# Performance work log

Measured on AMD Instinct MI355X. Metric: run time of the kernel, lower is better.

Reference implementation:

```python
import jax, jax.numpy as jnp
import numpy as np

NUM_CLASSES = 32768
FEAT_DIM = 512
BATCH = 1024


def setup_inputs() -> dict:
    key = jax.random.key(0)
    k1, k2, k3 = jax.random.split(key, 3)
    x = jax.random.normal(k1, (BATCH, FEAT_DIM), dtype=jnp.float32)
    labels = jax.random.randint(k2, (BATCH,), 0, NUM_CLASSES, dtype=jnp.int64)
    centers = jax.random.normal(k3, (NUM_CLASSES, FEAT_DIM), dtype=jnp.float32)
    return {"x": x, "labels": labels, "centers": centers}


def reference(x, labels, centers):
    # Original computes full cdist(x, centers)**2 / 2 and masks to the
    # label-matched column; mathematically identical to gathering each
    # sample's own center and taking half the squared L2 distance.
    c = centers[labels]                       # [B, D] gather
    diff = x - c                              # [B, D]
    per_sample = 0.5 * jnp.sum(diff * diff, axis=1)  # [B]
    return jnp.mean(per_sample)               # reduction='mean'
```

## Files before the change

kernel.cpp:

```cpp
#include <hip/hip_runtime.h>

#define BATCH 1024
#define FEAT_DIM 512
#define NBLK 128
#define MAGIC 0x5CA1AB1Eu

__global__ __launch_bounds__(256) void cl_fused(
    const float* __restrict__ x,
    const int* __restrict__ labels,
    const float* __restrict__ centers,
    float* __restrict__ partial,
    unsigned int* __restrict__ flags,
    float* __restrict__ out)
{
    const int wave = threadIdx.x >> 6;
    const int lane = threadIdx.x & 63;
    const int b0   = blockIdx.x * 8 + wave * 2;
    const int b1   = b0 + 1;

    const int lab0 = labels[b0];
    const int lab1 = labels[b1];

    const float4* __restrict__ x0 =
        reinterpret_cast<const float4*>(x + (size_t)b0 * FEAT_DIM);
    const float4* __restrict__ x1 =
        reinterpret_cast<const float4*>(x + (size_t)b1 * FEAT_DIM);
    const float4* __restrict__ c0 =
        reinterpret_cast<const float4*>(centers + (size_t)lab0 * FEAT_DIM);
    const float4* __restrict__ c1 =
        reinterpret_cast<const float4*>(centers + (size_t)lab1 * FEAT_DIM);

    const float4 xa = x0[lane];
    const float4 xb = x0[lane + 64];
    const float4 xc = x1[lane];
    const float4 xd = x1[lane + 64];
    const float4 ca = c0[lane];
    const float4 cb = c0[lane + 64];
    const float4 cc = c1[lane];
    const float4 cd = c1[lane + 64];

    float s;
    {
        const float e0 = xa.x - ca.x, e1 = xa.y - ca.y;
        const float e2 = xa.z - ca.z, e3 = xa.w - ca.w;
        const float e4 = xb.x - cb.x, e5 = xb.y - cb.y;
        const float e6 = xb.z - cb.z, e7 = xb.w - cb.w;
        const float f0 = xc.x - cc.x, f1 = xc.y - cc.y;
        const float f2 = xc.z - cc.z, f3 = xc.w - cc.w;
        const float f4 = xd.x - cd.x, f5 = xd.y - cd.y;
        const float f6 = xd.z - cd.z, f7 = xd.w - cd.w;
        s = e0 * e0 + e1 * e1 + e2 * e2 + e3 * e3
          + e4 * e4 + e5 * e5 + e6 * e6 + e7 * e7
          + f0 * f0 + f1 * f1 + f2 * f2 + f3 * f3
          + f4 * f4 + f5 * f5 + f6 * f6 + f7 * f7;
    }

    #pragma unroll
    for (int off = 32; off > 0; off >>= 1)
        s += __shfl_down(s, off, 64);

    __shared__ float wsum[4];
    if (lane == 0) wsum[wave] = s;
    __syncthreads();

    if (threadIdx.x == 0) {
        const float p = wsum[0] + wsum[1] + wsum[2] + wsum[3];
        __hip_atomic_store(&partial[blockIdx.x], p,
                           __ATOMIC_RELAXED, __HIP_MEMORY_SCOPE_AGENT);
        __hip_atomic_store(&flags[blockIdx.x], MAGIC,
                           __ATOMIC_RELEASE, __HIP_MEMORY_SCOPE_AGENT);
    }

    if (blockIdx.x == 0 && wave == 0) {
        const int i0 = lane, i1 = lane + 64;
        bool done = false;
        while (!__all(done)) {
            done = (__hip_atomic_load(&flags[i0], __ATOMIC_ACQUIRE,
                                      __HIP_MEMORY_SCOPE_AGENT) == MAGIC)
                && (__hip_atomic_load(&flags[i1], __ATOMIC_ACQUIRE,
                                      __HIP_MEMORY_SCOPE_AGENT) == MAGIC);
            if (!done) __builtin_amdgcn_s_sleep(2);
        }

        float t = __hip_atomic_load(&partial[i0], __ATOMIC_RELAXED,
                                    __HIP_MEMORY_SCOPE_AGENT)
                + __hip_atomic_load(&partial[i1], __ATOMIC_RELAXED,
                                    __HIP_MEMORY_SCOPE_AGENT);

        #pragma unroll
        for (int off = 32; off > 0; off >>= 1)
            t += __shfl_down(t, off, 64);

        if (lane == 0) out[0] = t * (0.5f / (float)BATCH);

        __hip_atomic_store(&flags[i0], 0u, __ATOMIC_RELAXED, __HIP_MEMORY_SCOPE_AGENT);
        __hip_atomic_store(&flags[i1], 0u, __ATOMIC_RELAXED, __HIP_MEMORY_SCOPE_AGENT);
    }
}

extern "C" void kernel_launch(void* const* d_in, const int* in_sizes, int n_in,
                              void* d_out, int out_size, void* d_ws, size_t ws_size,
                              hipStream_t stream) {
    const float* x       = (const float*)d_in[0];
    const int*   labels  = (const int*)d_in[1];
    const float* centers = (const float*)d_in[2];
    float*       out     = (float*)d_out;

    float*        partial = (float*)d_ws;
    unsigned int* flags   = (unsigned int*)((char*)d_ws + 1024);

    cl_fused<<<NBLK, 256, 0, stream>>>(x, labels, centers, partial, flags, out);
}
```

Before: 10.38 us.

## Use dedicated reducer block and 64 worker blocks with four samples per wave

```diff
diff --git a/kernel.cpp b/kernel.cpp
--- a/kernel.cpp
+++ b/kernel.cpp
@@ -2,7 +2,7 @@
 
 #define BATCH 1024
 #define FEAT_DIM 512
-#define NBLK 128
+#define NWORK 64
 #define MAGIC 0x5CA1AB1Eu
 
 __global__ __launch_bounds__(256) void cl_fused(
@@ -15,44 +15,85 @@
 {
     const int wave = threadIdx.x >> 6;
     const int lane = threadIdx.x & 63;
-    const int b0   = blockIdx.x * 8 + wave * 2;
-    const int b1   = b0 + 1;
+
+    if (blockIdx.x == 0) {
+        if (wave == 0) {
+            bool done = false;
+            while (!__all(done)) {
+                done = (__hip_atomic_load(&flags[lane], __ATOMIC_RELAXED,
+                                          __HIP_MEMORY_SCOPE_AGENT) == MAGIC);
+            }
+            __builtin_amdgcn_fence(__ATOMIC_ACQUIRE, "agent");
+
+            float t = __hip_atomic_load(&partial[lane], __ATOMIC_RELAXED,
+                                        __HIP_MEMORY_SCOPE_AGENT);
+            #pragma unroll
+            for (int off = 32; off > 0; off >>= 1)
+                t += __shfl_down(t, off, 64);
+
+            if (lane == 0) out[0] = t * (0.5f / (float)BATCH);
+
+            __hip_atomic_store(&flags[lane], 0u, __ATOMIC_RELAXED,
+                               __HIP_MEMORY_SCOPE_AGENT);
+        }
+        return;
+    }
+
+    const int blk = blockIdx.x - 1;
+    const int b0  = blk * 16 + wave * 4;
 
     const int lab0 = labels[b0];
-    const int lab1 = labels[b1];
+    const int lab1 = labels[b0 + 1];
+    const int lab2 = labels[b0 + 2];
+    const int lab3 = labels[b0 + 3];
 
-    const float4* __restrict__ x0 =
+    const float4* __restrict__ xr =
         reinterpret_cast<const float4*>(x + (size_t)b0 * FEAT_DIM);
-    const float4* __restrict__ x1 =
-        reinterpret_cast<const float4*>(x + (size_t)b1 * FEAT_DIM);
     const float4* __restrict__ c0 =
         reinterpret_cast<const float4*>(centers + (size_t)lab0 * FEAT_DIM);
     const float4* __restrict__ c1 =
         reinterpret_cast<const float4*>(centers + (size_t)lab1 * FEAT_DIM);
+    const float4* __restrict__ c2 =
+        reinterpret_cast<const float4*>(centers + (size_t)lab2 * FEAT_DIM);
+    const float4* __restrict__ c3 =
+        reinterpret_cast<const float4*>(centers + (size_t)lab3 * FEAT_DIM);
 
-    const float4 xa = x0[lane];
-    const float4 xb = x0[lane + 64];
-    const float4 xc = x1[lane];
-    const float4 xd = x1[lane + 64];
-    const float4 ca = c0[lane];
-    const float4 cb = c0[lane + 64];
-    const float4 cc = c1[lane];
-    const float4 cd = c1[lane + 64];
+    const float4 xa0 = xr[lane];
+    const float4 xa1 = xr[lane + 64];
+    const float4 xb0 = xr[lane + 128];
+    const float4 xb1 = xr[lane + 192];
+    const float4 xc0 = xr[lane + 256];
+    const float4 xc1 = xr[lane + 320];
+    const float4 xd0 = xr[lane + 384];
+    const float4 xd1 = xr[lane + 448];
+    const float4 ca0 = c0[lane];
+    const float4 ca1 = c0[lane + 64];
+    const float4 cb0 = c1[lane];
+    const float4 cb1 = c1[lane + 64];
+    const float4 cc0 = c2[lane];
+    const float4 cc1 = c2[lane + 64];
+    const float4 cd0 = c3[lane];
+    const float4 cd1 = c3[lane + 64];
 
-    float s;
+    float s = 0.f;
     {
-        const float e0 = xa.x - ca.x, e1 = xa.y - ca.y;
-        const float e2 = xa.z - ca.z, e3 = xa.w - ca.w;
-        const float e4 = xb.x - cb.x, e5 = xb.y - cb.y;
-        const float e6 = xb.z - cb.z, e7 = xb.w - cb.w;
-        const float f0 = xc.x - cc.x, f1 = xc.y - cc.y;
-        const float f2 = xc.z - cc.z, f3 = xc.w - cc.w;
-        const float f4 = xd.x - cd.x, f5 = xd.y - cd.y;
-        const float f6 = xd.z - cd.z, f7 = xd.w - cd.w;
-        s = e0 * e0 + e1 * e1 + e2 * e2 + e3 * e3
-          + e4 * e4 + e5 * e5 + e6 * e6 + e7 * e7
-          + f0 * f0 + f1 * f1 + f2 * f2 + f3 * f3
-          + f4 * f4 + f5 * f5 + f6 * f6 + f7 * f7;
+        float d;
+        d = xa0.x - ca0.x; s += d * d;  d = xa0.y - ca0.y; s += d * d;
+        d = xa0.z - ca0.z; s += d * d;  d = xa0.w - ca0.w; s += d * d;
+        d = xa1.x - ca1.x; s += d * d;  d = xa1.y - ca1.y; s += d * d;
+        d = xa1.z - ca1.z; s += d * d;  d = xa1.w - ca1.w; s += d * d;
+        d = xb0.x - cb0.x; s += d * d;  d = xb0.y - cb0.y; s += d * d;
+        d = xb0.z - cb0.z; s += d * d;  d = xb0.w - cb0.w; s += d * d;
+        d = xb1.x - cb1.x; s += d * d;  d = xb1.y - cb1.y; s += d * d;
+        d = xb1.z - cb1.z; s += d * d;  d = xb1.w - cb1.w; s += d * d;
+        d = xc0.x - cc0.x; s += d * d;  d = xc0.y - cc0.y; s += d * d;
+        d = xc0.z - cc0.z; s += d * d;  d = xc0.w - cc0.w; s += d * d;
+        d = xc1.x - cc1.x; s += d * d;  d = xc1.y - cc1.y; s += d * d;
+        d = xc1.z - cc1.z; s += d * d;  d = xc1.w - cc1.w; s += d * d;
+        d = xd0.x - cd0.x; s += d * d;  d = xd0.y - cd0.y; s += d * d;
+        d = xd0.z - cd0.z; s += d * d;  d = xd0.w - cd0.w; s += d * d;
+        d = xd1.x - cd1.x; s += d * d;  d = xd1.y - cd1.y; s += d * d;
+        d = xd1.z - cd1.z; s += d * d;  d = xd1.w - cd1.w; s += d * d;
     }
 
     #pragma unroll
@@ -65,36 +106,10 @@
 
     if (threadIdx.x == 0) {
         const float p = wsum[0] + wsum[1] + wsum[2] + wsum[3];
-        __hip_atomic_store(&partial[blockIdx.x], p,
+        __hip_atomic_store(&partial[blk], p,
                            __ATOMIC_RELAXED, __HIP_MEMORY_SCOPE_AGENT);
-        __hip_atomic_store(&flags[blockIdx.x], MAGIC,
+        __hip_atomic_store(&flags[blk], MAGIC,
                            __ATOMIC_RELEASE, __HIP_MEMORY_SCOPE_AGENT);
-    }
-
-    if (blockIdx.x == 0 && wave == 0) {
-        const int i0 = lane, i1 = lane + 64;
-        bool done = false;
-        while (!__all(done)) {
-            done = (__hip_atomic_load(&flags[i0], __ATOMIC_ACQUIRE,
-                                      __HIP_MEMORY_SCOPE_AGENT) == MAGIC)
-                && (__hip_atomic_load(&flags[i1], __ATOMIC_ACQUIRE,
-                                      __HIP_MEMORY_SCOPE_AGENT) == MAGIC);
-            if (!done) __builtin_amdgcn_s_sleep(2);
-        }
-
-        float t = __hip_atomic_load(&partial[i0], __ATOMIC_RELAXED,
-                                    __HIP_MEMORY_SCOPE_AGENT)
-                + __hip_atomic_load(&partial[i1], __ATOMIC_RELAXED,
-                                    __HIP_MEMORY_SCOPE_AGENT);
-
-        #pragma unroll
-        for (int off = 32; off > 0; off >>= 1)
-            t += __shfl_down(t, off, 64);
-
-        if (lane == 0) out[0] = t * (0.5f / (float)BATCH);
-
-        __hip_atomic_store(&flags[i0], 0u, __ATOMIC_RELAXED, __HIP_MEMORY_SCOPE_AGENT);
-        __hip_atomic_store(&flags[i1], 0u, __ATOMIC_RELAXED, __HIP_MEMORY_SCOPE_AGENT);
     }
 }
 
@@ -109,5 +124,5 @@
     float*        partial = (float*)d_ws;
     unsigned int* flags   = (unsigned int*)((char*)d_ws + 1024);
 
-    cl_fused<<<NBLK, 256, 0, stream>>>(x, labels, centers, partial, flags, out);
+    cl_fused<<<NWORK + 1, 256, 0, stream>>>(x, labels, centers, partial, flags, out);
 }
```

Result: faster. 9.739 us (-6.1%).
